# Kernel optimization log

Measured on AMD Instinct MI355X. Metric: run time of the kernel, lower is better.

The kernel has to match this reference:

```python
import jax, jax.numpy as jnp
import numpy as np

N_ENTS = 50000
N_EDGES = 500000
N_RELS = 200
RANK = 128
N_LAYERS = 2
RRELU_SLOPE = (1.0 / 8.0 + 1.0 / 3.0) / 2.0  # F.rrelu eval-mode: mean of default lower/upper


def setup_inputs() -> dict:
    key = jax.random.key(0)
    ks = jax.random.split(key, 9)
    return {
        "ent_emb": jax.random.normal(ks[0], (N_ENTS, RANK), dtype=jnp.float32),
        "rel_emb": jax.random.normal(ks[1], (N_RELS, RANK), dtype=jnp.float32),
        "norm": jax.random.uniform(ks[2], (N_ENTS, 1), dtype=jnp.float32),
        "Wn": jax.random.normal(ks[3], (N_LAYERS, RANK, RANK), dtype=jnp.float32) * 0.05,
        "Wl": jax.random.normal(ks[4], (N_LAYERS, RANK, RANK), dtype=jnp.float32) * 0.05,
        "Wa": jax.random.normal(ks[5], (N_LAYERS, RANK, RANK), dtype=jnp.float32) * 0.05,
        "src": jax.random.randint(ks[6], (N_EDGES,), 0, N_ENTS, dtype=jnp.int32),
        "dst": jax.random.randint(ks[7], (N_EDGES,), 0, N_ENTS, dtype=jnp.int32),
        "etype": jax.random.randint(ks[8], (N_EDGES,), 0, N_RELS, dtype=jnp.int32),
    }


def reference(ent_emb, rel_emb, norm, Wn, Wl, Wa, src, dst, etype):
    n = ent_emb.shape[0]
    # in-degree mask (same graph across layers)
    in_deg = jax.ops.segment_sum(jnp.ones_like(dst, dtype=jnp.float32), dst, num_segments=n)
    has_in = (in_deg > 0)[:, None]  # [N,1]
    h = ent_emb
    for l in range(Wn.shape[0]):
        # edge gather + add + linear: msg = (h[src] + rel_emb[etype]) @ Wn[l]
        msg = (h[src] + rel_emb[etype]) @ Wn[l]  # [E, rank]
        # scatter-sum into destination nodes, then per-node norm
        agg = jax.ops.segment_sum(msg, dst, num_segments=n) * norm  # [N, rank]
        # masked self-loop: loop_weight where in_degree>0, else alone_loop_weight
        loop = jnp.where(has_in, h @ Wl[l], h @ Wa[l])
        h = agg + loop
        # rrelu in eval mode == leaky relu with slope (1/8 + 1/3)/2
        h = jnp.where(h >= 0, h, h * RRELU_SLOPE)
        # dropout=0.0 -> identity
    return h
```

## Files before the change

kernel.cpp:

```cpp
#include <hip/hip_runtime.h>

#define SLOPE 0.22916666666666666f
#define ALONE_CAP 2048

typedef __attribute__((ext_vector_type(8))) short bfrag;
typedef __attribute__((ext_vector_type(4))) float ffrag;

__device__ __forceinline__ unsigned short rne16(float f) {
    unsigned u = __float_as_uint(f);
    return (unsigned short)((u + 0x7FFFu + ((u >> 16) & 1u)) >> 16);
}
__device__ __forceinline__ float bf2f(unsigned short h) {
    return __uint_as_float(((unsigned)h) << 16);
}
__device__ __forceinline__ unsigned packsplit(float f) {
    unsigned short hi = rne16(f);
    unsigned short lo = rne16(f - bf2f(hi));
    return ((unsigned)hi << 16) | lo;
}
__device__ __forceinline__ float recon(unsigned u) {
    return __uint_as_float(u & 0xFFFF0000u) + __uint_as_float(u << 16);
}
__device__ __forceinline__ float4 recon4(uint4 u) {
    return make_float4(recon(u.x), recon(u.y), recon(u.z), recon(u.w));
}

__global__ __launch_bounds__(256) void prep_kernel(
    const int* __restrict__ dst, int* __restrict__ deg, int e, int eb,
    const float* __restrict__ ent, unsigned* __restrict__ Esp,
    int total4, int cb,
    const float* __restrict__ Wn, const float* __restrict__ Wl,
    ushort* __restrict__ packW) {
    int b = blockIdx.x;
    if (b < eb) {
        int i = b * 256 + threadIdx.x;
        if (i < e) atomicAdd(&deg[dst[i]], 1);
    } else if (b < eb + cb) {
        int i = (b - eb) * 256 + threadIdx.x;
        if (i >= total4) return;
        float4 v = ((const float4*)ent)[i];
        uint4 w;
        w.x = packsplit(v.x); w.y = packsplit(v.y);
        w.z = packsplit(v.z); w.w = packsplit(v.w);
        ((uint4*)Esp)[i] = w;
    } else {
        int t = (b - eb - cb) * 256 + threadIdx.x;
        if (t >= 4 * 4 * 128 * 4) return;
        int quad = t & 3;
        int nn   = (t >> 2) & 127;
        int kc   = (t >> 9) & 3;
        int mat  = t >> 11;
        const float* W = ((mat & 1) ? Wl : Wn) + (mat >> 1) * 16384;
        ushort* oh = packW + mat * 32768;
        ushort* ol = oh + 16384;
        int obase = ((kc * 128 + nn) * 4 + quad) * 8;
        #pragma unroll
        for (int j = 0; j < 8; ++j) {
            float w = W[(kc * 32 + quad * 8 + j) * 128 + nn];
            unsigned short hi = rne16(w);
            oh[obase + j] = hi;
            ol[obase + j] = rne16(w - bf2f(hi));
        }
    }
}

__global__ __launch_bounds__(256) void scan_partial_kernel(const int* __restrict__ deg,
                                                           int* __restrict__ partial, int n) {
    __shared__ int wsum[4];
    int base = blockIdx.x * 1024;
    int t = threadIdx.x;
    int s = 0;
    #pragma unroll
    for (int j = 0; j < 4; ++j) {
        int i = base + t + 256 * j;
        if (i < n) s += deg[i];
    }
    #pragma unroll
    for (int off = 1; off < 64; off <<= 1) s += __shfl_xor(s, off, 64);
    if ((t & 63) == 0) wsum[t >> 6] = s;
    __syncthreads();
    if (t == 0) partial[blockIdx.x] = wsum[0] + wsum[1] + wsum[2] + wsum[3];
}

__global__ __launch_bounds__(256) void scan_final_kernel(const int* __restrict__ deg,
                                                         const int* __restrict__ partial,
                                                         int* __restrict__ row_off,
                                                         int* __restrict__ alone_list,
                                                         int* __restrict__ alone_count, int n) {
    __shared__ int wsum[4];
    __shared__ int sbase;
    int bid = blockIdx.x;
    int t = threadIdx.x, lane = t & 63, wid = t >> 6;
    if (wid == 0) {
        int v = (lane < bid) ? partial[lane] : 0;
        #pragma unroll
        for (int off = 1; off < 64; off <<= 1) v += __shfl_xor(v, off, 64);
        if (lane == 0) sbase = v;
    }
    int base = bid * 1024;
    int i0 = base + t * 4;
    int v0 = (i0 + 0 < n) ? deg[i0 + 0] : 0;
    int v1 = (i0 + 1 < n) ? deg[i0 + 1] : 0;
    int v2 = (i0 + 2 < n) ? deg[i0 + 2] : 0;
    int v3 = (i0 + 3 < n) ? deg[i0 + 3] : 0;
    int s = v0 + v1 + v2 + v3;
    int x = s;
    #pragma unroll
    for (int off = 1; off < 64; off <<= 1) {
        int y = __shfl_up(x, off, 64);
        if (lane >= off) x += y;
    }
    if (lane == 63) wsum[wid] = x;
    __syncthreads();
    int wbase = 0;
    #pragma unroll
    for (int w = 0; w < 4; ++w) { int ws = wsum[w]; if (w < wid) wbase += ws; }
    int p = sbase + wbase + x - s;
    if (i0 + 0 <= n) row_off[i0 + 0] = p;
    p += v0;
    if (i0 + 1 <= n) row_off[i0 + 1] = p;
    p += v1;
    if (i0 + 2 <= n) row_off[i0 + 2] = p;
    p += v2;
    if (i0 + 3 <= n) row_off[i0 + 3] = p;
    if (i0 + 0 < n && v0 == 0) { int q = atomicAdd(alone_count, 1); if (q < ALONE_CAP) alone_list[q] = i0; }
    if (i0 + 1 < n && v1 == 0) { int q = atomicAdd(alone_count, 1); if (q < ALONE_CAP) alone_list[q] = i0 + 1; }
    if (i0 + 2 < n && v2 == 0) { int q = atomicAdd(alone_count, 1); if (q < ALONE_CAP) alone_list[q] = i0 + 2; }
    if (i0 + 3 < n && v3 == 0) { int q = atomicAdd(alone_count, 1); if (q < ALONE_CAP) alone_list[q] = i0 + 3; }
}

__global__ __launch_bounds__(256) void scatter_kernel(
    const int* __restrict__ src, const int* __restrict__ dst,
    const int* __restrict__ ety, const int* __restrict__ row_off,
    int* __restrict__ cursor, unsigned* __restrict__ edges, int e) {
    int i = blockIdx.x * 256 + threadIdx.x;
    if (i < e) {
        int v = dst[i];
        int pos = row_off[v] + atomicAdd(&cursor[v], 1);
        edges[pos] = (unsigned)src[i] | ((unsigned)ety[i] << 16);
    }
}

template <int SPLIT>
__global__ __launch_bounds__(256) void agg_kernel(
    const float* __restrict__ hf, const unsigned* __restrict__ hs,
    const float* __restrict__ rel,
    const float* __restrict__ norm, const int* __restrict__ row_off,
    const unsigned* __restrict__ edges, unsigned* __restrict__ Ssp, int n) {
    int wave = threadIdx.x >> 6, lane = threadIdx.x & 63;
    int v = blockIdx.x * 4 + wave;
    if (v >= n) return;
    int s0 = row_off[v], s1 = row_off[v + 1];
    float nm = norm[v];
    int half = lane >> 5;
    int c4 = (lane & 31) * 4;
    float4 acc = make_float4(0.f, 0.f, 0.f, 0.f);
    int e = s0;
    for (; e + 7 < s1; e += 8) {
        unsigned q0 = edges[e + half];
        unsigned q1 = edges[e + 2 + half];
        unsigned q2 = edges[e + 4 + half];
        unsigned q3 = edges[e + 6 + half];
        float4 h0, h1, h2, h3;
        if (SPLIT) {
            h0 = recon4(*(const uint4*)&hs[(size_t)(q0 & 0xFFFFu) * 128 + c4]);
            h1 = recon4(*(const uint4*)&hs[(size_t)(q1 & 0xFFFFu) * 128 + c4]);
            h2 = recon4(*(const uint4*)&hs[(size_t)(q2 & 0xFFFFu) * 128 + c4]);
            h3 = recon4(*(const uint4*)&hs[(size_t)(q3 & 0xFFFFu) * 128 + c4]);
        } else {
            h0 = *(const float4*)&hf[(size_t)(q0 & 0xFFFFu) * 128 + c4];
            h1 = *(const float4*)&hf[(size_t)(q1 & 0xFFFFu) * 128 + c4];
            h2 = *(const float4*)&hf[(size_t)(q2 & 0xFFFFu) * 128 + c4];
            h3 = *(const float4*)&hf[(size_t)(q3 & 0xFFFFu) * 128 + c4];
        }
        float4 r0 = *(const float4*)&rel[(size_t)(q0 >> 16) * 128 + c4];
        float4 r1 = *(const float4*)&rel[(size_t)(q1 >> 16) * 128 + c4];
        float4 r2 = *(const float4*)&rel[(size_t)(q2 >> 16) * 128 + c4];
        float4 r3 = *(const float4*)&rel[(size_t)(q3 >> 16) * 128 + c4];
        acc.x += ((h0.x + r0.x) + (h1.x + r1.x)) + ((h2.x + r2.x) + (h3.x + r3.x));
        acc.y += ((h0.y + r0.y) + (h1.y + r1.y)) + ((h2.y + r2.y) + (h3.y + r3.y));
        acc.z += ((h0.z + r0.z) + (h1.z + r1.z)) + ((h2.z + r2.z) + (h3.z + r3.z));
        acc.w += ((h0.w + r0.w) + (h1.w + r1.w)) + ((h2.w + r2.w) + (h3.w + r3.w));
    }
    for (; e + 1 < s1; e += 2) {
        unsigned q0 = edges[e + half];
        float4 h0 = SPLIT ? recon4(*(const uint4*)&hs[(size_t)(q0 & 0xFFFFu) * 128 + c4])
                          : *(const float4*)&hf[(size_t)(q0 & 0xFFFFu) * 128 + c4];
        float4 r0 = *(const float4*)&rel[(size_t)(q0 >> 16) * 128 + c4];
        acc.x += h0.x + r0.x; acc.y += h0.y + r0.y;
        acc.z += h0.z + r0.z; acc.w += h0.w + r0.w;
    }
    if (e < s1 && half == 0) {
        unsigned q0 = edges[e];
        float4 h0 = SPLIT ? recon4(*(const uint4*)&hs[(size_t)(q0 & 0xFFFFu) * 128 + c4])
                          : *(const float4*)&hf[(size_t)(q0 & 0xFFFFu) * 128 + c4];
        float4 r0 = *(const float4*)&rel[(size_t)(q0 >> 16) * 128 + c4];
        acc.x += h0.x + r0.x; acc.y += h0.y + r0.y;
        acc.z += h0.z + r0.z; acc.w += h0.w + r0.w;
    }
    acc.x += __shfl_xor(acc.x, 32, 64);
    acc.y += __shfl_xor(acc.y, 32, 64);
    acc.z += __shfl_xor(acc.z, 32, 64);
    acc.w += __shfl_xor(acc.w, 32, 64);
    if (half == 0) {
        uint4 w;
        w.x = packsplit(acc.x * nm); w.y = packsplit(acc.y * nm);
        w.z = packsplit(acc.z * nm); w.w = packsplit(acc.w * nm);
        *(uint4*)&Ssp[(size_t)v * 128 + c4] = w;
    }
}

__global__ __launch_bounds__(256, 3) void gemm_mfma_kernel(
    const unsigned* __restrict__ Ssp, const unsigned* Hsp,
    const ushort* __restrict__ Pnh, const ushort* __restrict__ Pnl,
    const ushort* __restrict__ Plh, const ushort* __restrict__ Pll,
    float* __restrict__ out, unsigned* Osp, int n) {
    const int tid = threadIdx.x;
    const int wave = tid >> 6, lane = tid & 63;
    const int quad = lane >> 4, l16 = lane & 15;
    const int row_base = blockIdx.x * 64 + wave * 16;

    int r0c = row_base + l16;
    if (r0c > n - 1) r0c = n - 1;
    const size_t arow = (size_t)r0c * 128;

    ffrag acc[8];
    #pragma unroll
    for (int ct = 0; ct < 8; ++ct) acc[ct] = (ffrag)0.f;

    uint4 a_cur0 = *(const uint4*)(Ssp + arow + quad * 8);
    uint4 a_cur1 = *(const uint4*)(Ssp + arow + quad * 8 + 4);

    #pragma unroll 1
    for (int it = 0; it < 8; ++it) {
        const int kc = it & 3;
        const ushort* Pbh = (it >= 4) ? Plh : Pnh;
        const ushort* Pbl = (it >= 4) ? Pll : Pnl;

        uint4 a_nxt0, a_nxt1;
        if (it < 7) {
            const unsigned* An = (it + 1 >= 4) ? Hsp : Ssp;
            const int koffn = ((it + 1) & 3) * 32 + quad * 8;
            a_nxt0 = *(const uint4*)(An + arow + koffn);
            a_nxt1 = *(const uint4*)(An + arow + koffn + 4);
        }

        bfrag bh[8], bl[8];
        #pragma unroll
        for (int ct = 0; ct < 8; ++ct) {
            int bidx = ((kc * 128 + ct * 16 + l16) * 4 + quad) * 8;
            bh[ct] = *(const bfrag*)(Pbh + bidx);
            bl[ct] = *(const bfrag*)(Pbl + bidx);
        }

        bfrag ah, al;
        #pragma unroll
        for (int j = 0; j < 4; ++j) {
            unsigned u0 = ((const unsigned*)&a_cur0)[j];
            unsigned u1 = ((const unsigned*)&a_cur1)[j];
            ah[j]     = (short)(u0 >> 16); al[j]     = (short)(u0 & 0xFFFFu);
            ah[j + 4] = (short)(u1 >> 16); al[j + 4] = (short)(u1 & 0xFFFFu);
        }

        #pragma unroll
        for (int ct = 0; ct < 8; ++ct)
            acc[ct] = __builtin_amdgcn_mfma_f32_16x16x32_bf16(ah, bh[ct], acc[ct], 0, 0, 0);
        #pragma unroll
        for (int ct = 0; ct < 8; ++ct)
            acc[ct] = __builtin_amdgcn_mfma_f32_16x16x32_bf16(ah, bl[ct], acc[ct], 0, 0, 0);
        #pragma unroll
        for (int ct = 0; ct < 8; ++ct)
            acc[ct] = __builtin_amdgcn_mfma_f32_16x16x32_bf16(al, bh[ct], acc[ct], 0, 0, 0);

        a_cur0 = a_nxt0;
        a_cur1 = a_nxt1;
    }

    #pragma unroll
    for (int ct = 0; ct < 8; ++ct) {
        #pragma unroll
        for (int rg = 0; rg < 4; ++rg) {
            int r = row_base + quad * 4 + rg;
            if (r < n) {
                int c = ct * 16 + l16;
                float v = acc[ct][rg];
                v = v >= 0.f ? v : v * SLOPE;
                if (out) out[(size_t)r * 128 + c] = v;
                if (Osp) Osp[(size_t)r * 128 + c] = packsplit(v);
            }
        }
    }
}

__global__ __launch_bounds__(128) void fixup_kernel(
    const float* __restrict__ Hrows, int by_node,
    const float* __restrict__ Wa,
    const int* __restrict__ alone_list, const int* __restrict__ alone_count,
    float* out, unsigned* Osp, float* asave) {
    int cnt = *alone_count;
    if (cnt > ALONE_CAP) cnt = ALONE_CAP;
    int t = threadIdx.x;
    for (int i = blockIdx.x; i < cnt; i += gridDim.x) {
        int v = alone_list[i];
        const float* hrow = Hrows + (size_t)(by_node ? v : i) * 128;
        float acc = 0.f;
        for (int k = 0; k < 128; ++k)
            acc += hrow[k] * Wa[k * 128 + t];
        float o = acc >= 0.f ? acc : acc * SLOPE;
        if (out) out[(size_t)v * 128 + t] = o;
        if (Osp) Osp[(size_t)v * 128 + t] = packsplit(o);
        if (asave) asave[(size_t)i * 128 + t] = o;
    }
}

extern "C" void kernel_launch(void* const* d_in, const int* in_sizes, int n_in,
                              void* d_out, int out_size, void* d_ws, size_t ws_size,
                              hipStream_t stream) {
    const float* ent  = (const float*)d_in[0];
    const float* rel  = (const float*)d_in[1];
    const float* norm = (const float*)d_in[2];
    const float* Wn   = (const float*)d_in[3];
    const float* Wl   = (const float*)d_in[4];
    const float* Wa   = (const float*)d_in[5];
    const int*   src  = (const int*)d_in[6];
    const int*   dst  = (const int*)d_in[7];
    const int*   ety  = (const int*)d_in[8];
    float* out = (float*)d_out;

    const int n = in_sizes[2];
    const int e = in_sizes[7];

    char* ws = (char*)d_ws;
    int* deg         = (int*)ws;
    int* cursor      = deg + n;
    int* alone_count = cursor + n;
    size_t zbytes = (size_t)(2 * n + 1) * sizeof(int);
    size_t p = (zbytes + 255) & ~(size_t)255;
    int* row_off = (int*)(ws + p);
    p += (((size_t)(n + 1) * 4) + 255) & ~(size_t)255;
    int* partial = (int*)(ws + p);
    p += 256;
    int* alone_list = (int*)(ws + p);
    p += (((size_t)ALONE_CAP * 4) + 255) & ~(size_t)255;
    float* asave = (float*)(ws + p);
    p += (((size_t)ALONE_CAP * 128 * 4) + 255) & ~(size_t)255;
    unsigned* edges = (unsigned*)(ws + p);
    p += (((size_t)e * 4) + 255) & ~(size_t)255;
    unsigned* Ssp = (unsigned*)(ws + p);
    p += (((size_t)n * 128 * 4) + 255) & ~(size_t)255;
    unsigned* Esp = (unsigned*)(ws + p);
    p += (((size_t)n * 128 * 4) + 255) & ~(size_t)255;
    ushort* packW = (ushort*)(ws + p);
    p += 4 * 32768 * 2;

    const int eb = (e + 255) / 256;
    const int cb = (n * 32 + 255) / 256;
    const int nparts = (n + 1023) / 1024;
    const int gb = (n + 63) / 64;
    const int ab = (n + 3) / 4;

    hipMemsetAsync(ws, 0, zbytes, stream);
    prep_kernel<<<eb + cb + 32, 256, 0, stream>>>(dst, deg, e, eb,
                                                  ent, Esp, n * 32, cb,
                                                  Wn, Wl, packW);
    scan_partial_kernel<<<nparts, 256, 0, stream>>>(deg, partial, n);
    scan_final_kernel<<<nparts, 256, 0, stream>>>(deg, partial, row_off,
                                                  alone_list, alone_count, n);
    scatter_kernel<<<eb, 256, 0, stream>>>(src, dst, ety, row_off, cursor, edges, e);

    agg_kernel<0><<<ab, 256, 0, stream>>>(ent, nullptr, rel, norm, row_off, edges, Ssp, n);
    gemm_mfma_kernel<<<gb, 256, 0, stream>>>(Ssp, Esp,
                                             packW, packW + 16384,
                                             packW + 32768, packW + 49152,
                                             nullptr, Esp, n);
    fixup_kernel<<<16, 128, 0, stream>>>(ent, 1, Wa, alone_list, alone_count,
                                         nullptr, Esp, asave);

    agg_kernel<1><<<ab, 256, 0, stream>>>(nullptr, Esp, rel, norm, row_off, edges, Ssp, n);
    gemm_mfma_kernel<<<gb, 256, 0, stream>>>(Ssp, Esp,
                                             packW + 65536, packW + 81920,
                                             packW + 98304, packW + 114688,
                                             out, nullptr, n);
    fixup_kernel<<<16, 128, 0, stream>>>(asave, 0, Wa + 16384, alone_list, alone_count,
                                         out, nullptr, nullptr);
}
```

Before: 316.5 us.

## Stage packed weight tiles in double-buffered LDS and preload all A fragments

Reorders the packed weight layout so each k-chunk is a contiguous lane-ordered 4096-element tile. The GEMM kernel now copies each tile cooperatively into a double-buffered LDS array and overlaps the next tile's global load with the current MFMAs, instead of every wave reading B fragments from global memory. All eight A fragments are loaded up front, and occupancy is lowered from 3 to 2 blocks per SM to make room for the extra registers and LDS. This trades added barriers and register pressure for less redundant global and L2 traffic on the weights.

```diff
diff --git a/kernel.cpp b/kernel.cpp
--- a/kernel.cpp
+++ b/kernel.cpp
@@ -53,7 +53,7 @@
         const float* W = ((mat & 1) ? Wl : Wn) + (mat >> 1) * 16384;
         ushort* oh = packW + mat * 32768;
         ushort* ol = oh + 16384;
-        int obase = ((kc * 128 + nn) * 4 + quad) * 8;
+        int obase = kc * 4096 + (nn >> 4) * 512 + (quad * 16 + (nn & 15)) * 8;
         #pragma unroll
         for (int j = 0; j < 8; ++j) {
             float w = W[(kc * 32 + quad * 8 + j) * 128 + nn];
@@ -210,11 +210,13 @@
     }
 }
 
-__global__ __launch_bounds__(256, 3) void gemm_mfma_kernel(
+__global__ __launch_bounds__(256, 2) void gemm_mfma_kernel(
     const unsigned* __restrict__ Ssp, const unsigned* Hsp,
     const ushort* __restrict__ Pnh, const ushort* __restrict__ Pnl,
     const ushort* __restrict__ Plh, const ushort* __restrict__ Pll,
     float* __restrict__ out, unsigned* Osp, int n) {
+    __shared__ ushort ldsB[2][2][4096];
+
     const int tid = threadIdx.x;
     const int wave = tid >> 6, lane = tid & 63;
     const int quad = lane >> 4, l16 = lane & 15;
@@ -223,58 +225,90 @@
     int r0c = row_base + l16;
     if (r0c > n - 1) r0c = n - 1;
     const size_t arow = (size_t)r0c * 128;
+    const int q8 = quad * 8;
 
     ffrag acc[8];
     #pragma unroll
     for (int ct = 0; ct < 8; ++ct) acc[ct] = (ffrag)0.f;
 
-    uint4 a_cur0 = *(const uint4*)(Ssp + arow + quad * 8);
-    uint4 a_cur1 = *(const uint4*)(Ssp + arow + quad * 8 + 4);
-
-    #pragma unroll 1
-    for (int it = 0; it < 8; ++it) {
-        const int kc = it & 3;
-        const ushort* Pbh = (it >= 4) ? Plh : Pnh;
-        const ushort* Pbl = (it >= 4) ? Pll : Pnl;
-
-        uint4 a_nxt0, a_nxt1;
-        if (it < 7) {
-            const unsigned* An = (it + 1 >= 4) ? Hsp : Ssp;
-            const int koffn = ((it + 1) & 3) * 32 + quad * 8;
-            a_nxt0 = *(const uint4*)(An + arow + koffn);
-            a_nxt1 = *(const uint4*)(An + arow + koffn + 4);
-        }
-
-        bfrag bh[8], bl[8];
-        #pragma unroll
-        for (int ct = 0; ct < 8; ++ct) {
-            int bidx = ((kc * 128 + ct * 16 + l16) * 4 + quad) * 8;
-            bh[ct] = *(const bfrag*)(Pbh + bidx);
-            bl[ct] = *(const bfrag*)(Pbl + bidx);
-        }
-
-        bfrag ah, al;
-        #pragma unroll
-        for (int j = 0; j < 4; ++j) {
-            unsigned u0 = ((const unsigned*)&a_cur0)[j];
-            unsigned u1 = ((const unsigned*)&a_cur1)[j];
-            ah[j]     = (short)(u0 >> 16); al[j]     = (short)(u0 & 0xFFFFu);
-            ah[j + 4] = (short)(u1 >> 16); al[j + 4] = (short)(u1 & 0xFFFFu);
-        }
-
-        #pragma unroll
-        for (int ct = 0; ct < 8; ++ct)
-            acc[ct] = __builtin_amdgcn_mfma_f32_16x16x32_bf16(ah, bh[ct], acc[ct], 0, 0, 0);
-        #pragma unroll
-        for (int ct = 0; ct < 8; ++ct)
-            acc[ct] = __builtin_amdgcn_mfma_f32_16x16x32_bf16(ah, bl[ct], acc[ct], 0, 0, 0);
-        #pragma unroll
-        for (int ct = 0; ct < 8; ++ct)
-            acc[ct] = __builtin_amdgcn_mfma_f32_16x16x32_bf16(al, bh[ct], acc[ct], 0, 0, 0);
-
-        a_cur0 = a_nxt0;
-        a_cur1 = a_nxt1;
-    }
+    uint4 a00 = *(const uint4*)(Ssp + arow + 0 * 32 + q8);
+    uint4 a01 = *(const uint4*)(Ssp + arow + 0 * 32 + q8 + 4);
+    uint4 a10 = *(const uint4*)(Ssp + arow + 1 * 32 + q8);
+    uint4 a11 = *(const uint4*)(Ssp + arow + 1 * 32 + q8 + 4);
+    uint4 a20 = *(const uint4*)(Ssp + arow + 2 * 32 + q8);
+    uint4 a21 = *(const uint4*)(Ssp + arow + 2 * 32 + q8 + 4);
+    uint4 a30 = *(const uint4*)(Ssp + arow + 3 * 32 + q8);
+    uint4 a31 = *(const uint4*)(Ssp + arow + 3 * 32 + q8 + 4);
+    uint4 a40 = *(const uint4*)(Hsp + arow + 0 * 32 + q8);
+    uint4 a41 = *(const uint4*)(Hsp + arow + 0 * 32 + q8 + 4);
+    uint4 a50 = *(const uint4*)(Hsp + arow + 1 * 32 + q8);
+    uint4 a51 = *(const uint4*)(Hsp + arow + 1 * 32 + q8 + 4);
+    uint4 a60 = *(const uint4*)(Hsp + arow + 2 * 32 + q8);
+    uint4 a61 = *(const uint4*)(Hsp + arow + 2 * 32 + q8 + 4);
+    uint4 a70 = *(const uint4*)(Hsp + arow + 3 * 32 + q8);
+    uint4 a71 = *(const uint4*)(Hsp + arow + 3 * 32 + q8 + 4);
+    {
+        uint4 t0 = *(const uint4*)(Pnh + tid * 8);
+        uint4 t1 = *(const uint4*)(Pnh + 2048 + tid * 8);
+        uint4 t2 = *(const uint4*)(Pnl + tid * 8);
+        uint4 t3 = *(const uint4*)(Pnl + 2048 + tid * 8);
+        *(uint4*)&ldsB[0][0][tid * 8] = t0;
+        *(uint4*)&ldsB[0][0][2048 + tid * 8] = t1;
+        *(uint4*)&ldsB[0][1][tid * 8] = t2;
+        *(uint4*)&ldsB[0][1][2048 + tid * 8] = t3;
+    }
+    __syncthreads();
+
+#define GSTEP(IT, A0, A1, NPH, NPL, NKC, HAVE)                                   \
+    {                                                                            \
+        uint4 s0, s1, s2, s3;                                                    \
+        if (HAVE) {                                                              \
+            s0 = *(const uint4*)((NPH) + (NKC) * 4096 + tid * 8);                \
+            s1 = *(const uint4*)((NPH) + (NKC) * 4096 + 2048 + tid * 8);         \
+            s2 = *(const uint4*)((NPL) + (NKC) * 4096 + tid * 8);                \
+            s3 = *(const uint4*)((NPL) + (NKC) * 4096 + 2048 + tid * 8);         \
+        }                                                                        \
+        bfrag bh[8], bl[8];                                                      \
+        _Pragma("unroll")                                                        \
+        for (int ct = 0; ct < 8; ++ct) {                                         \
+            bh[ct] = *(const bfrag*)&ldsB[(IT) & 1][0][ct * 512 + lane * 8];     \
+            bl[ct] = *(const bfrag*)&ldsB[(IT) & 1][1][ct * 512 + lane * 8];     \
+        }                                                                        \
+        bfrag ah, al;                                                            \
+        _Pragma("unroll")                                                        \
+        for (int j = 0; j < 4; ++j) {                                            \
+            unsigned u0 = ((const unsigned*)&(A0))[j];                           \
+            unsigned u1 = ((const unsigned*)&(A1))[j];                           \
+            ah[j]     = (short)(u0 >> 16); al[j]     = (short)(u0 & 0xFFFFu);    \
+            ah[j + 4] = (short)(u1 >> 16); al[j + 4] = (short)(u1 & 0xFFFFu);    \
+        }                                                                        \
+        _Pragma("unroll")                                                        \
+        for (int ct = 0; ct < 8; ++ct)                                           \
+            acc[ct] = __builtin_amdgcn_mfma_f32_16x16x32_bf16(ah, bh[ct], acc[ct], 0, 0, 0); \
+        _Pragma("unroll")                                                        \
+        for (int ct = 0; ct < 8; ++ct)                                           \
+            acc[ct] = __builtin_amdgcn_mfma_f32_16x16x32_bf16(ah, bl[ct], acc[ct], 0, 0, 0); \
+        _Pragma("unroll")                                                        \
+        for (int ct = 0; ct < 8; ++ct)                                           \
+            acc[ct] = __builtin_amdgcn_mfma_f32_16x16x32_bf16(al, bh[ct], acc[ct], 0, 0, 0); \
+        if (HAVE) {                                                              \
+            *(uint4*)&ldsB[((IT) + 1) & 1][0][tid * 8] = s0;                     \
+            *(uint4*)&ldsB[((IT) + 1) & 1][0][2048 + tid * 8] = s1;              \
+            *(uint4*)&ldsB[((IT) + 1) & 1][1][tid * 8] = s2;                     \
+            *(uint4*)&ldsB[((IT) + 1) & 1][1][2048 + tid * 8] = s3;              \
+            __syncthreads();                                                     \
+        }                                                                        \
+    }
+
+    GSTEP(0, a00, a01, Pnh, Pnl, 1, 1)
+    GSTEP(1, a10, a11, Pnh, Pnl, 2, 1)
+    GSTEP(2, a20, a21, Pnh, Pnl, 3, 1)
+    GSTEP(3, a30, a31, Plh, Pll, 0, 1)
+    GSTEP(4, a40, a41, Plh, Pll, 1, 1)
+    GSTEP(5, a50, a51, Plh, Pll, 2, 1)
+    GSTEP(6, a60, a61, Plh, Pll, 3, 1)
+    GSTEP(7, a70, a71, Plh, Pll, 0, 0)
+#undef GSTEP
 
     #pragma unroll
     for (int ct = 0; ct < 8; ++ct) {
```

Measured after the change: 282.5 us. -10.7%, faster.
